# Kernel optimization log

Hardware: AMD Instinct MI355X
Metric: run time of the kernel (lower is better)

Reference implementation:

```python
import jax, jax.numpy as jnp
import numpy as np

B, C, H, W = 8, 256, 128, 128
N = H * W
TEMP = 0.07
NUM_NEG = 128
HARD_RADIUS = 4
HARD_RATIO = 0.75   # curriculum fully ramped (_current_hard_ratio == hard_ratio_max)
N_HARD = int(NUM_NEG * HARD_RATIO)   # 96
N_RAND = NUM_NEG - N_HARD            # 32
STEP = max(1, H // 16)               # 8
N_POS = ((H + STEP - 1) // STEP) * ((W + STEP - 1) // STEP)  # 256


def setup_inputs() -> dict:
    key = jax.random.key(0)
    ks = jax.random.split(key, 8)
    fmap_rgb = jax.random.normal(ks[0], (B, C, H, W), jnp.float32)
    fmap_depth = jax.random.normal(ks[1], (B, C, H, W), jnp.float32)
    pu = jax.random.uniform(ks[2], (B, H, W), jnp.float32) * (W - 1)
    pv = jax.random.uniform(ks[3], (B, H, W), jnp.float32) * (H - 1)
    projected_coords = jnp.stack([pu, pv], axis=1)  # (B,2,H,W)
    valid_mask = (jax.random.uniform(ks[4], (B, H, W)) < 0.9).astype(jnp.float32)
    rand_idx = jax.random.randint(ks[5], (B, N_RAND), 0, N, dtype=jnp.int32)
    hard_off_u = jax.random.randint(ks[6], (B, N_HARD, N_POS), -HARD_RADIUS, HARD_RADIUS + 1, dtype=jnp.int32)
    hard_off_v = jax.random.randint(ks[7], (B, N_HARD, N_POS), -HARD_RADIUS, HARD_RADIUS + 1, dtype=jnp.int32)
    return {
        'fmap_rgb': fmap_rgb, 'fmap_depth': fmap_depth,
        'projected_coords': projected_coords, 'valid_mask': valid_mask,
        'rand_idx': rand_idx, 'hard_off_u': hard_off_u, 'hard_off_v': hard_off_v,
    }


def _normalize(x):
    # F.normalize(dim=1): x / max(||x||_2, eps)
    n = jnp.sqrt(jnp.sum(x * x, axis=1, keepdims=True))
    return x / jnp.maximum(n, 1e-12)


def _bilinear_sample(f, x, y):
    # grid_sample(mode=bilinear, padding=zeros, align_corners=True); unnormalized
    # coords equal pixel coords (x=proj_u, y=proj_v). f:(B,C,H,W), x,y:(B,H,W) -> (B,C,N)
    Bb, Cc, Hh, Ww = f.shape
    ff = f.reshape(Bb, Cc, Hh * Ww)
    xf = x.reshape(Bb, -1)
    yf = y.reshape(Bb, -1)
    x0 = jnp.floor(xf)
    y0 = jnp.floor(yf)
    wx = xf - x0
    wy = yf - y0
    x0i = x0.astype(jnp.int32)
    y0i = y0.astype(jnp.int32)

    def g(ix, iy):
        valid = (ix >= 0) & (ix < Ww) & (iy >= 0) & (iy < Hh)
        idx = jnp.clip(iy, 0, Hh - 1) * Ww + jnp.clip(ix, 0, Ww - 1)
        v = jnp.take_along_axis(ff, idx[:, None, :], axis=2)
        return v * valid[:, None, :]

    return (((1 - wx) * (1 - wy))[:, None, :] * g(x0i, y0i)
            + (wx * (1 - wy))[:, None, :] * g(x0i + 1, y0i)
            + ((1 - wx) * wy)[:, None, :] * g(x0i, y0i + 1)
            + (wx * wy)[:, None, :] * g(x0i + 1, y0i + 1))


def reference(fmap_rgb, fmap_depth, projected_coords, valid_mask, rand_idx, hard_off_u, hard_off_v):
    rgb = _normalize(fmap_rgb)
    dep = _normalize(fmap_depth)
    proj_u = projected_coords[:, 0]
    proj_v = projected_coords[:, 1]

    rgb_pos = _bilinear_sample(rgb, proj_u, proj_v)        # (B,C,N)
    dep_flat = dep.reshape(B, C, N)
    rgb_flat = rgb.reshape(B, C, N)
    pos_sim = jnp.sum(dep_flat * rgb_pos, axis=1) / TEMP    # (B,N)

    # random negatives via gather + batched matmul
    rgb_rand = jnp.take_along_axis(rgb_flat, rand_idx[:, None, :].astype(jnp.int32), axis=2)  # (B,C,n_rand)
    rand_neg = jnp.einsum('bcn,bck->bkn', dep_flat, rgb_rand) / TEMP  # (B,n_rand,N)

    # hard negatives on coarse grid (step = H//16)
    gh = jnp.arange(0, H, STEP)
    gw = jnp.arange(0, W, STEP)
    ghf, gwf = [a.reshape(-1) for a in jnp.meshgrid(gh, gw, indexing='ij')]
    grid_idx = ghf * W + gwf                                # (n_pos,)
    pos_u = jnp.clip(proj_u[:, ghf, gwf], 0, W - 1).astype(jnp.int32)  # (B,n_pos)
    pos_v = jnp.clip(proj_v[:, ghf, gwf], 0, H - 1).astype(jnp.int32)
    off_u = jnp.where((hard_off_u == 0) & (hard_off_v == 0), 1, hard_off_u)
    hu = jnp.clip(pos_u[:, None, :] + off_u, 0, W - 1)      # (B,n_hard,n_pos)
    hv = jnp.clip(pos_v[:, None, :] + hard_off_v, 0, H - 1)
    hard_idx = (hv * W + hu).reshape(B, -1)                 # (B, n_hard*n_pos)
    rgb_hard = jnp.take_along_axis(rgb_flat, hard_idx[:, None, :], axis=2).reshape(B, C, N_HARD, N_POS)
    dep_grid = dep_flat[:, :, grid_idx]                     # (B,C,n_pos)
    hard_sim = jnp.einsum('bcp,bchp->bhp', dep_grid, rgb_hard) / TEMP  # (B,n_hard,n_pos)

    # logsumexp over [pos; random negs; hard negs] -- hard negs only exist at grid
    # positions (the torch code scatters into a dense -inf (B,n_hard,N) tensor;
    # logaddexp at grid positions is mathematically identical and avoids it).
    lse_base = jax.scipy.special.logsumexp(
        jnp.concatenate([pos_sim[:, None, :], rand_neg], axis=1), axis=1)  # (B,N)
    lse_hard = jax.scipy.special.logsumexp(hard_sim, axis=1)               # (B,n_pos)
    lse = lse_base.at[:, grid_idx].set(jnp.logaddexp(lse_base[:, grid_idx], lse_hard))

    mask = valid_mask.reshape(B, N)
    denom = jnp.maximum(jnp.sum(mask), 1.0)
    loss = jnp.sum((lse - pos_sim) * mask) / denom

    # accuracy (no_grad in torch); max over all negatives, hard ones only at grid idx
    max_neg = jnp.max(rand_neg, axis=1)
    max_neg = max_neg.at[:, grid_idx].max(jnp.max(hard_sim, axis=1))
    correct = ((pos_sim > max_neg) & (mask > 0.5)).astype(jnp.float32)
    accuracy = jnp.sum(correct) / denom * 100.0
    return loss, jax.lax.stop_gradient(accuracy)
```

## Files before the change

### kernel.cpp

```cpp
#include <hip/hip_runtime.h>
#include <cfloat>
#include <math.h>

#define B_ 8
#define C_ 256
#define C2_ (C_/2)
#define H_ 128
#define W_ 128
#define N_ (H_*W_)
#define NRAND 32
#define NHARD 96
#define NPOS 256
#define INV_TEMP (1.0f/0.07f)

typedef __attribute__((ext_vector_type(8))) short short8;
typedef __attribute__((ext_vector_type(4))) float f32x4;

__device__ __forceinline__ unsigned bf16rne(float x) {
    unsigned u = __float_as_uint(x);
    return (u + 0x7FFFu + ((u >> 16) & 1u)) >> 16;
}
__device__ __forceinline__ float blo(unsigned w) { return __uint_as_float(w << 16); }
__device__ __forceinline__ float bhi(unsigned w) { return __uint_as_float(w & 0xFFFF0000u); }

__global__ __launch_bounds__(256) void k1_rgb_norm_T(const float* __restrict__ rgb,
                                                     unsigned* __restrict__ rgbT) {
    __shared__ __align__(16) uint4 bounce[64 * 32];
    __shared__ float red[4][64];
    __shared__ float invn[64];
    int bi = blockIdx.x;
    int b  = bi >> 8;
    int p0 = (bi & 255) << 6;
    int t  = threadIdx.x;
    int lane = t & 63, w = t >> 6;

    const float* src = rgb + (size_t)b * C_ * N_ + p0 + lane;
    float v[64];
    float ssq = 0.f;
    #pragma unroll
    for (int k = 0; k < 64; ++k) {
        v[k] = src[(size_t)(w * 64 + k) * N_];
        ssq += v[k] * v[k];
    }
    red[w][lane] = ssq;
    __syncthreads();
    if (t < 64) {
        float s = red[0][t] + red[1][t] + red[2][t] + red[3][t];
        invn[t] = 1.0f / fmaxf(sqrtf(s), 1e-12f);
    }
    __syncthreads();
    float sc = invn[lane];
    int swz = lane & 7;
    #pragma unroll
    for (int j = 0; j < 8; ++j) {
        uint4 q;
        q.x = bf16rne(v[8 * j + 0] * sc) | (bf16rne(v[8 * j + 1] * sc) << 16);
        q.y = bf16rne(v[8 * j + 2] * sc) | (bf16rne(v[8 * j + 3] * sc) << 16);
        q.z = bf16rne(v[8 * j + 4] * sc) | (bf16rne(v[8 * j + 5] * sc) << 16);
        q.w = bf16rne(v[8 * j + 6] * sc) | (bf16rne(v[8 * j + 7] * sc) << 16);
        bounce[lane * 32 + ((w * 8 + j) ^ swz)] = q;
    }
    __syncthreads();
    uint4* dst = (uint4*)(rgbT + (size_t)(b * N_ + p0) * C2_);
    #pragma unroll
    for (int it = 0; it < 8; ++it) {
        int idx = it * 256 + t;
        int px = idx >> 5, j = idx & 31;
        dst[idx] = bounce[px * 32 + (j ^ (px & 7))];
    }
}

__global__ __launch_bounds__(256) void k2_main(
        const float* __restrict__ dep, const unsigned* __restrict__ rgbT,
        const float* __restrict__ coords, const int* __restrict__ rand_idx,
        float* __restrict__ lse_base, float* __restrict__ pos_out,
        float* __restrict__ maxneg_out, unsigned* __restrict__ depG) {
    __shared__ __align__(16) uint4 dep4[64 * 32];
    __shared__ __align__(16) uint4 rs4[32 * 32];
    __shared__ float red[4][64];
    __shared__ float invn[64];
    int bi = blockIdx.x;
    int b  = bi >> 8;
    int p0 = (bi & 255) << 6;
    int t  = threadIdx.x;
    int lane = t & 63, w = t >> 6;

    #pragma unroll
    for (int it = 0; it < 4; ++it) {
        int flat = it * 256 + t;
        int rn = flat >> 5, c8 = flat & 31;
        int idx = rand_idx[b * NRAND + rn];
        const uint4* src = (const uint4*)(rgbT + (size_t)(b * N_ + idx) * C2_);
        rs4[rn * 32 + (c8 ^ (rn & 7))] = src[c8];
    }

    const float* depb = dep + (size_t)b * C_ * N_ + p0 + lane;
    float ssq = 0.f;
    int psw = lane & 7;
    #pragma unroll 2
    for (int i = 0; i < 8; ++i) {
        int c0 = w * 64 + i * 8;
        float v[8];
        #pragma unroll
        for (int k = 0; k < 8; ++k) {
            v[k] = depb[(size_t)(c0 + k) * N_];
            ssq += v[k] * v[k];
        }
        uint4 q;
        q.x = bf16rne(v[0]) | (bf16rne(v[1]) << 16);
        q.y = bf16rne(v[2]) | (bf16rne(v[3]) << 16);
        q.z = bf16rne(v[4]) | (bf16rne(v[5]) << 16);
        q.w = bf16rne(v[6]) | (bf16rne(v[7]) << 16);
        dep4[lane * 32 + ((w * 8 + i) ^ psw)] = q;
    }
    red[w][lane] = ssq;

    int px = t >> 2, g = t & 3;
    int n  = p0 + px;
    float xf = coords[(size_t)b * 2 * N_ + n];
    float yf = coords[(size_t)b * 2 * N_ + N_ + n];
    float x0 = floorf(xf), y0 = floorf(yf);
    float wx = xf - x0, wy = yf - y0;
    int ix = (int)x0 + (g & 1);
    int iy = (int)y0 + (g >> 1);
    float wgt = ((g & 1) ? wx : 1.f - wx) * ((g & 2) ? wy : 1.f - wy);
    if (ix < 0 || ix >= W_ || iy < 0 || iy >= H_) wgt = 0.f;
    int ixc = min(max(ix, 0), W_ - 1), iyc = min(max(iy, 0), H_ - 1);
    const uint4* nbr4 = (const uint4*)(rgbT + (size_t)(b * N_ + iyc * W_ + ixc) * C2_);

    __syncthreads();
    if (t < 64) {
        float s = red[0][t] + red[1][t] + red[2][t] + red[3][t];
        invn[t] = 1.0f / fmaxf(sqrtf(s), 1e-12f);
    }

    f32x4 acc0 = {0.f, 0.f, 0.f, 0.f};
    f32x4 acc1 = {0.f, 0.f, 0.f, 0.f};
    int l15 = lane & 15, l4 = lane >> 4;
    int pxA = (w << 4) + l15;
    const short8* lds8 = (const short8*)dep4;
    const short8* rnd8 = (const short8*)rs4;
    #pragma unroll
    for (int kc = 0; kc < 8; ++kc) {
        int c8 = kc * 4 + l4;
        short8 a  = lds8[pxA * 32 + (c8 ^ (pxA & 7))];
        short8 b0 = rnd8[l15 * 32 + (c8 ^ (l15 & 7))];
        short8 b1 = rnd8[(16 + l15) * 32 + (c8 ^ (l15 & 7))];
        acc0 = __builtin_amdgcn_mfma_f32_16x16x32_bf16(a, b0, acc0, 0, 0, 0);
        acc1 = __builtin_amdgcn_mfma_f32_16x16x32_bf16(a, b1, acc1, 0, 0, 0);
    }

    float accN = 0.f;
    const uint4* drow = dep4 + (size_t)px * 32;
    int dsw = px & 7;
    #pragma unroll 4
    for (int c8 = 0; c8 < 32; ++c8) {
        uint4 dq = drow[c8 ^ dsw];
        uint4 rq = nbr4[c8];
        accN += blo(dq.x) * blo(rq.x) + bhi(dq.x) * bhi(rq.x)
              + blo(dq.y) * blo(rq.y) + bhi(dq.y) * bhi(rq.y)
              + blo(dq.z) * blo(rq.z) + bhi(dq.z) * bhi(rq.z)
              + blo(dq.w) * blo(rq.w) + bhi(dq.w) * bhi(rq.w);
    }
    __syncthreads();

    float* simsF = (float*)rs4;
    #pragma unroll
    for (int r = 0; r < 4; ++r) {
        int prow = (w << 4) + (l4 << 2) + r;
        int swn = r << 2;
        simsF[prow * 32 + (l15 ^ swn)]        = acc0[r];
        simsF[prow * 32 + (16 + (l15 ^ swn))] = acc1[r];
    }
    __syncthreads();

    float scale = invn[px] * INV_TEMP;
    float pp = accN * wgt;
    pp += __shfl_xor(pp, 1, 4);
    pp += __shfl_xor(pp, 2, 4);
    float pos = pp * scale;
    const float4* sf = (const float4*)simsF;
    int fsw = px & 3;
    float4 ra = sf[px * 8 + ((g * 2) ^ fsw)];
    float4 rb = sf[px * 8 + (((g * 2) ^ fsw) ^ 1)];
    float r[8] = {ra.x, ra.y, ra.z, ra.w, rb.x, rb.y, rb.z, rb.w};
    float ml = -FLT_MAX;
    #pragma unroll
    for (int j = 0; j < 8; ++j) { r[j] *= scale; ml = fmaxf(ml, r[j]); }
    ml = fmaxf(ml, __shfl_xor(ml, 1, 4));
    ml = fmaxf(ml, __shfl_xor(ml, 2, 4));
    float mneg = ml;
    float mall = fmaxf(mneg, pos);
    float se = 0.f;
    #pragma unroll
    for (int j = 0; j < 8; ++j) se += expf(r[j] - mall);
    se += __shfl_xor(se, 1, 4);
    se += __shfl_xor(se, 2, 4);
    if (g == 0) {
        float lse = mall + logf(se + expf(pos - mall));
        size_t o = (size_t)b * N_ + n;
        lse_base[o]   = lse;
        pos_out[o]    = pos;
        maxneg_out[o] = mneg;
    }

    int y = p0 >> 7;
    if ((y & 7) == 0) {
        int m = t >> 5, u = t & 31;
        int gpx = m * 8;
        int gx  = (p0 & 127) + gpx;
        int p   = ((y >> 3) << 4) + (gx >> 3);
        float sc = invn[gpx];
        const unsigned* srow = (const unsigned*)(dep4 + (size_t)gpx * 32);
        int xsw = (gpx & 7) << 2;
        unsigned* dst = depG + (size_t)((b << 8) + p) * 128;
        #pragma unroll
        for (int it = 0; it < 4; ++it) {
            int uu = u + it * 32;
            unsigned wv = srow[uu ^ xsw];
            dst[uu] = bf16rne(blo(wv) * sc) | (bf16rne(bhi(wv) * sc) << 16);
        }
    }
}

__global__ __launch_bounds__(192) void k3_hard(
        const unsigned* __restrict__ depG, const unsigned* __restrict__ rgbT,
        const float* __restrict__ coords, const int* __restrict__ hoffu,
        const int* __restrict__ hoffv, float* __restrict__ lse_hard,
        float* __restrict__ max_hard) {
    __shared__ __align__(16) float dv[256];
    __shared__ float sm_[3], ss_[3];
    int bp = blockIdx.x;
    int b = bp >> 8, p = bp & 255;
    int gy = (p >> 4) * 8, gx = (p & 15) * 8;
    int nn = gy * W_ + gx;
    int t  = threadIdx.x;
    if (t < 128) {
        unsigned wv = depG[(size_t)bp * 128 + t];
        dv[2 * t]     = blo(wv);
        dv[2 * t + 1] = bhi(wv);
    }
    float pu = coords[(size_t)b * 2 * N_ + nn];
    float pv = coords[(size_t)b * 2 * N_ + N_ + nn];
    int iu = (int)fminf(fmaxf(pu, 0.f), (float)(W_ - 1));
    int iv = (int)fminf(fmaxf(pv, 0.f), (float)(H_ - 1));
    int h = t >> 1, half = t & 1;
    int ou = hoffu[((size_t)b * NHARD + h) * NPOS + p];
    int ov = hoffv[((size_t)b * NHARD + h) * NPOS + p];
    __syncthreads();
    if (ou == 0 && ov == 0) ou = 1;
    int hu = min(max(iu + ou, 0), W_ - 1);
    int hv = min(max(iv + ov, 0), H_ - 1);
    const uint4* hvec = (const uint4*)(rgbT + (size_t)(b * N_ + hv * W_ + hu) * C2_)
                        + half * 16;
    const float4* dvv = (const float4*)dv + half * 32;
    float acc = 0.f;
    #pragma unroll 4
    for (int c8 = 0; c8 < 16; ++c8) {
        uint4 q = hvec[c8];
        float4 d0 = dvv[c8 * 2];
        float4 d1 = dvv[c8 * 2 + 1];
        acc += d0.x * blo(q.x) + d0.y * bhi(q.x)
             + d0.z * blo(q.y) + d0.w * bhi(q.y)
             + d1.x * blo(q.z) + d1.y * bhi(q.z)
             + d1.z * blo(q.w) + d1.w * bhi(q.w);
    }
    float sim = (acc + __shfl_xor(acc, 1, 2)) * INV_TEMP;
    float m = sim;
    #pragma unroll
    for (int o = 32; o > 0; o >>= 1) m = fmaxf(m, __shfl_xor(m, o, 64));
    int wid = t >> 6;
    if ((t & 63) == 0) sm_[wid] = m;
    __syncthreads();
    float mm = fmaxf(fmaxf(sm_[0], sm_[1]), sm_[2]);
    float e = (half == 0) ? expf(sim - mm) : 0.f;
    #pragma unroll
    for (int o = 32; o > 0; o >>= 1) e += __shfl_xor(e, o, 64);
    if ((t & 63) == 0) ss_[wid] = e;
    __syncthreads();
    if (t == 0) {
        lse_hard[bp] = mm + logf(ss_[0] + ss_[1] + ss_[2]);
        max_hard[bp] = mm;
    }
}

__global__ __launch_bounds__(256) void k4_reduce(
        const float* __restrict__ lse_base, const float* __restrict__ pos_sim,
        const float* __restrict__ max_neg, const float* __restrict__ mask,
        const float* __restrict__ lse_hard, const float* __restrict__ max_hard,
        float* __restrict__ acc) {
    int i = blockIdx.x * 256 + threadIdx.x;
    float l  = lse_base[i], ps = pos_sim[i], mn = max_neg[i], mk = mask[i];
    int b = i >> 14;
    int n = i & (N_ - 1);
    int y = n >> 7, x = n & 127;
    if (((y & 7) | (x & 7)) == 0) {
        int p = ((y >> 3) << 4) + (x >> 3);
        float lh = lse_hard[(b << 8) + p];
        float mh = max_hard[(b << 8) + p];
        float m = fmaxf(l, lh);
        l  = m + logf(expf(l - m) + expf(lh - m));
        mn = fmaxf(mn, mh);
    }
    float s0 = (l - ps) * mk;
    float s1 = (ps > mn && mk > 0.5f) ? 1.f : 0.f;
    float s2 = mk;
    #pragma unroll
    for (int o = 32; o > 0; o >>= 1) {
        s0 += __shfl_down(s0, o, 64);
        s1 += __shfl_down(s1, o, 64);
        s2 += __shfl_down(s2, o, 64);
    }
    __shared__ float r0[4], r1[4], r2[4];
    int wid = threadIdx.x >> 6;
    if ((threadIdx.x & 63) == 0) { r0[wid] = s0; r1[wid] = s1; r2[wid] = s2; }
    __syncthreads();
    if (threadIdx.x == 0) {
        atomicAdd(&acc[0], r0[0] + r0[1] + r0[2] + r0[3]);
        atomicAdd(&acc[1], r1[0] + r1[1] + r1[2] + r1[3]);
        atomicAdd(&acc[2], r2[0] + r2[1] + r2[2] + r2[3]);
    }
}

__global__ void k5_final(const float* __restrict__ acc, float* __restrict__ out) {
    if (threadIdx.x == 0) {
        float denom = fmaxf(acc[2], 1.0f);
        out[0] = acc[0] / denom;
        out[1] = acc[1] / denom * 100.0f;
    }
}

extern "C" void kernel_launch(void* const* d_in, const int* in_sizes, int n_in,
                              void* d_out, int out_size, void* d_ws, size_t ws_size,
                              hipStream_t stream) {
    const float* rgb     = (const float*)d_in[0];
    const float* dep     = (const float*)d_in[1];
    const float* coords  = (const float*)d_in[2];
    const float* mask    = (const float*)d_in[3];
    const int*   rand_i  = (const int*)d_in[4];
    const int*   hoffu   = (const int*)d_in[5];
    const int*   hoffv   = (const int*)d_in[6];
    float* out = (float*)d_out;
    char*  ws  = (char*)d_ws;

    const size_t RGBT_B = (size_t)B_ * N_ * C_ * 2;
    const size_t PIX_B  = (size_t)B_ * N_ * 4;
    unsigned* rgbT  = (unsigned*)ws;
    float* lse_base = (float*)(ws + RGBT_B);
    float* pos_sim  = (float*)(ws + RGBT_B + PIX_B);
    float* max_neg  = (float*)(ws + RGBT_B + 2 * PIX_B);
    float* lse_hard = (float*)(ws + RGBT_B + 3 * PIX_B);
    float* max_hard = (float*)(ws + RGBT_B + 3 * PIX_B + 8192);
    float* acc      = (float*)(ws + RGBT_B + 3 * PIX_B + 2 * 8192);
    unsigned* depG  = (unsigned*)(ws + RGBT_B + 3 * PIX_B + 2 * 8192 + 1024);

    hipMemsetAsync(acc, 0, 16, stream);
    k1_rgb_norm_T<<<B_ * (N_ / 64), 256, 0, stream>>>(rgb, rgbT);
    k2_main<<<B_ * (N_ / 64), 256, 0, stream>>>(dep, rgbT, coords, rand_i,
                                                lse_base, pos_sim, max_neg, depG);
    k3_hard<<<B_ * NPOS, 192, 0, stream>>>(depG, rgbT, coords, hoffu, hoffv,
                                           lse_hard, max_hard);
    k4_reduce<<<(B_ * N_) / 256, 256, 0, stream>>>(lse_base, pos_sim, max_neg,
                                                   mask, lse_hard, max_hard, acc);
    k5_final<<<1, 64, 0, stream>>>(acc, out);
}
```

Baseline: 371.8 us.

## Normalize depth features in first kernel and consume pre-transposed bf16 depth in main

```diff
diff --git a/kernel.cpp b/kernel.cpp
--- a/kernel.cpp
+++ b/kernel.cpp
@@ -23,18 +23,22 @@
 __device__ __forceinline__ float blo(unsigned w) { return __uint_as_float(w << 16); }
 __device__ __forceinline__ float bhi(unsigned w) { return __uint_as_float(w & 0xFFFF0000u); }
 
-__global__ __launch_bounds__(256) void k1_rgb_norm_T(const float* __restrict__ rgb,
-                                                     unsigned* __restrict__ rgbT) {
+__global__ __launch_bounds__(256, 4) void kA_norm(
+        const float* __restrict__ rgb, const float* __restrict__ dep,
+        unsigned* __restrict__ rgbT, unsigned* __restrict__ depT) {
     __shared__ __align__(16) uint4 bounce[64 * 32];
     __shared__ float red[4][64];
     __shared__ float invn[64];
     int bi = blockIdx.x;
-    int b  = bi >> 8;
-    int p0 = (bi & 255) << 6;
+    int srcsel = bi >> 11;
+    int sub = bi & 2047;
+    int b  = sub >> 8;
+    int p0 = (sub & 255) << 6;
     int t  = threadIdx.x;
     int lane = t & 63, w = t >> 6;
 
-    const float* src = rgb + (size_t)b * C_ * N_ + p0 + lane;
+    const float* src = (srcsel ? dep : rgb) + (size_t)b * C_ * N_ + p0 + lane;
+    unsigned* dstT = srcsel ? depT : rgbT;
     float v[64];
     float ssq = 0.f;
     #pragma unroll
@@ -61,7 +65,7 @@
         bounce[lane * 32 + ((w * 8 + j) ^ swz)] = q;
     }
     __syncthreads();
-    uint4* dst = (uint4*)(rgbT + (size_t)(b * N_ + p0) * C2_);
+    uint4* dst = (uint4*)(dstT + (size_t)(b * N_ + p0) * C2_);
     #pragma unroll
     for (int it = 0; it < 8; ++it) {
         int idx = it * 256 + t;
@@ -70,20 +74,18 @@
     }
 }
 
-__global__ __launch_bounds__(256) void k2_main(
-        const float* __restrict__ dep, const unsigned* __restrict__ rgbT,
+__global__ __launch_bounds__(256, 4) void k2_main(
+        const unsigned* __restrict__ depT, const unsigned* __restrict__ rgbT,
         const float* __restrict__ coords, const int* __restrict__ rand_idx,
         float* __restrict__ lse_base, float* __restrict__ pos_out,
-        float* __restrict__ maxneg_out, unsigned* __restrict__ depG) {
-    __shared__ __align__(16) uint4 dep4[64 * 32];
+        float* __restrict__ maxneg_out) {
     __shared__ __align__(16) uint4 rs4[32 * 32];
-    __shared__ float red[4][64];
-    __shared__ float invn[64];
     int bi = blockIdx.x;
     int b  = bi >> 8;
     int p0 = (bi & 255) << 6;
     int t  = threadIdx.x;
     int lane = t & 63, w = t >> 6;
+    int l15 = lane & 15, l4 = lane >> 4;
 
     #pragma unroll
     for (int it = 0; it < 4; ++it) {
@@ -94,26 +96,10 @@
         rs4[rn * 32 + (c8 ^ (rn & 7))] = src[c8];
     }
 
-    const float* depb = dep + (size_t)b * C_ * N_ + p0 + lane;
-    float ssq = 0.f;
-    int psw = lane & 7;
-    #pragma unroll 2
-    for (int i = 0; i < 8; ++i) {
-        int c0 = w * 64 + i * 8;
-        float v[8];
-        #pragma unroll
-        for (int k = 0; k < 8; ++k) {
-            v[k] = depb[(size_t)(c0 + k) * N_];
-            ssq += v[k] * v[k];
-        }
-        uint4 q;
-        q.x = bf16rne(v[0]) | (bf16rne(v[1]) << 16);
-        q.y = bf16rne(v[2]) | (bf16rne(v[3]) << 16);
-        q.z = bf16rne(v[4]) | (bf16rne(v[5]) << 16);
-        q.w = bf16rne(v[6]) | (bf16rne(v[7]) << 16);
-        dep4[lane * 32 + ((w * 8 + i) ^ psw)] = q;
-    }
-    red[w][lane] = ssq;
+    const short8* arow = (const short8*)(depT + (size_t)(b * N_ + p0 + (w << 4) + l15) * C2_);
+    short8 afr[8];
+    #pragma unroll
+    for (int kc = 0; kc < 8; ++kc) afr[kc] = arow[kc * 4 + l4];
 
     int px = t >> 2, g = t & 3;
     int n  = p0 + px;
@@ -129,33 +115,24 @@
     const uint4* nbr4 = (const uint4*)(rgbT + (size_t)(b * N_ + iyc * W_ + ixc) * C2_);
 
     __syncthreads();
-    if (t < 64) {
-        float s = red[0][t] + red[1][t] + red[2][t] + red[3][t];
-        invn[t] = 1.0f / fmaxf(sqrtf(s), 1e-12f);
-    }
 
     f32x4 acc0 = {0.f, 0.f, 0.f, 0.f};
     f32x4 acc1 = {0.f, 0.f, 0.f, 0.f};
-    int l15 = lane & 15, l4 = lane >> 4;
-    int pxA = (w << 4) + l15;
-    const short8* lds8 = (const short8*)dep4;
     const short8* rnd8 = (const short8*)rs4;
     #pragma unroll
     for (int kc = 0; kc < 8; ++kc) {
         int c8 = kc * 4 + l4;
-        short8 a  = lds8[pxA * 32 + (c8 ^ (pxA & 7))];
         short8 b0 = rnd8[l15 * 32 + (c8 ^ (l15 & 7))];
         short8 b1 = rnd8[(16 + l15) * 32 + (c8 ^ (l15 & 7))];
-        acc0 = __builtin_amdgcn_mfma_f32_16x16x32_bf16(a, b0, acc0, 0, 0, 0);
-        acc1 = __builtin_amdgcn_mfma_f32_16x16x32_bf16(a, b1, acc1, 0, 0, 0);
+        acc0 = __builtin_amdgcn_mfma_f32_16x16x32_bf16(afr[kc], b0, acc0, 0, 0, 0);
+        acc1 = __builtin_amdgcn_mfma_f32_16x16x32_bf16(afr[kc], b1, acc1, 0, 0, 0);
     }
 
     float accN = 0.f;
-    const uint4* drow = dep4 + (size_t)px * 32;
-    int dsw = px & 7;
+    const uint4* drow = (const uint4*)(depT + (size_t)(b * N_ + n) * C2_);
     #pragma unroll 4
     for (int c8 = 0; c8 < 32; ++c8) {
-        uint4 dq = drow[c8 ^ dsw];
+        uint4 dq = drow[c8];
         uint4 rq = nbr4[c8];
         accN += blo(dq.x) * blo(rq.x) + bhi(dq.x) * bhi(rq.x)
               + blo(dq.y) * blo(rq.y) + bhi(dq.y) * bhi(rq.y)
@@ -174,7 +151,7 @@
     }
     __syncthreads();
 
-    float scale = invn[px] * INV_TEMP;
+    const float scale = INV_TEMP;
     float pp = accN * wgt;
     pp += __shfl_xor(pp, 1, 4);
     pp += __shfl_xor(pp, 2, 4);
@@ -203,28 +180,10 @@
         pos_out[o]    = pos;
         maxneg_out[o] = mneg;
     }
-
-    int y = p0 >> 7;
-    if ((y & 7) == 0) {
-        int m = t >> 5, u = t & 31;
-        int gpx = m * 8;
-        int gx  = (p0 & 127) + gpx;
-        int p   = ((y >> 3) << 4) + (gx >> 3);
-        float sc = invn[gpx];
-        const unsigned* srow = (const unsigned*)(dep4 + (size_t)gpx * 32);
-        int xsw = (gpx & 7) << 2;
-        unsigned* dst = depG + (size_t)((b << 8) + p) * 128;
-        #pragma unroll
-        for (int it = 0; it < 4; ++it) {
-            int uu = u + it * 32;
-            unsigned wv = srow[uu ^ xsw];
-            dst[uu] = bf16rne(blo(wv) * sc) | (bf16rne(bhi(wv) * sc) << 16);
-        }
-    }
 }
 
 __global__ __launch_bounds__(192) void k3_hard(
-        const unsigned* __restrict__ depG, const unsigned* __restrict__ rgbT,
+        const unsigned* __restrict__ depT, const unsigned* __restrict__ rgbT,
         const float* __restrict__ coords, const int* __restrict__ hoffu,
         const int* __restrict__ hoffv, float* __restrict__ lse_hard,
         float* __restrict__ max_hard) {
@@ -236,7 +195,7 @@
     int nn = gy * W_ + gx;
     int t  = threadIdx.x;
     if (t < 128) {
-        unsigned wv = depG[(size_t)bp * 128 + t];
+        unsigned wv = depT[(size_t)(b * N_ + nn) * C2_ + t];
         dv[2 * t]     = blo(wv);
         dv[2 * t + 1] = bhi(wv);
     }
@@ -346,19 +305,19 @@
     const size_t RGBT_B = (size_t)B_ * N_ * C_ * 2;
     const size_t PIX_B  = (size_t)B_ * N_ * 4;
     unsigned* rgbT  = (unsigned*)ws;
-    float* lse_base = (float*)(ws + RGBT_B);
-    float* pos_sim  = (float*)(ws + RGBT_B + PIX_B);
-    float* max_neg  = (float*)(ws + RGBT_B + 2 * PIX_B);
-    float* lse_hard = (float*)(ws + RGBT_B + 3 * PIX_B);
-    float* max_hard = (float*)(ws + RGBT_B + 3 * PIX_B + 8192);
-    float* acc      = (float*)(ws + RGBT_B + 3 * PIX_B + 2 * 8192);
-    unsigned* depG  = (unsigned*)(ws + RGBT_B + 3 * PIX_B + 2 * 8192 + 1024);
+    unsigned* depT  = (unsigned*)(ws + RGBT_B);
+    float* lse_base = (float*)(ws + 2 * RGBT_B);
+    float* pos_sim  = (float*)(ws + 2 * RGBT_B + PIX_B);
+    float* max_neg  = (float*)(ws + 2 * RGBT_B + 2 * PIX_B);
+    float* lse_hard = (float*)(ws + 2 * RGBT_B + 3 * PIX_B);
+    float* max_hard = (float*)(ws + 2 * RGBT_B + 3 * PIX_B + 8192);
+    float* acc      = (float*)(ws + 2 * RGBT_B + 3 * PIX_B + 2 * 8192);
 
     hipMemsetAsync(acc, 0, 16, stream);
-    k1_rgb_norm_T<<<B_ * (N_ / 64), 256, 0, stream>>>(rgb, rgbT);
-    k2_main<<<B_ * (N_ / 64), 256, 0, stream>>>(dep, rgbT, coords, rand_i,
-                                                lse_base, pos_sim, max_neg, depG);
-    k3_hard<<<B_ * NPOS, 192, 0, stream>>>(depG, rgbT, coords, hoffu, hoffv,
+    kA_norm<<<2 * B_ * (N_ / 64), 256, 0, stream>>>(rgb, dep, rgbT, depT);
+    k2_main<<<B_ * (N_ / 64), 256, 0, stream>>>(depT, rgbT, coords, rand_i,
+                                                lse_base, pos_sim, max_neg);
+    k3_hard<<<B_ * NPOS, 192, 0, stream>>>(depT, rgbT, coords, hoffu, hoffv,
                                            lse_hard, max_hard);
     k4_reduce<<<(B_ * N_) / 256, 256, 0, stream>>>(lse_base, pos_sim, max_neg,
                                                    mask, lse_hard, max_hard, acc);
```

Measured after the change: 415.5 us. 11.7% more time.

## Fuse hard-negative scoring into main kernel and finalize via last-block reduction

Applied to the files above, without the earlier changes.

```diff
diff --git a/kernel.cpp b/kernel.cpp
--- a/kernel.cpp
+++ b/kernel.cpp
@@ -73,8 +73,10 @@
 __global__ __launch_bounds__(256) void k2_main(
         const float* __restrict__ dep, const unsigned* __restrict__ rgbT,
         const float* __restrict__ coords, const int* __restrict__ rand_idx,
+        const int* __restrict__ hoffu, const int* __restrict__ hoffv,
         float* __restrict__ lse_base, float* __restrict__ pos_out,
-        float* __restrict__ maxneg_out, unsigned* __restrict__ depG) {
+        float* __restrict__ maxneg_out, float* __restrict__ lse_hard,
+        float* __restrict__ max_hard) {
     __shared__ __align__(16) uint4 dep4[64 * 32];
     __shared__ __align__(16) uint4 rs4[32 * 32];
     __shared__ float red[4][64];
@@ -204,83 +206,64 @@
         maxneg_out[o] = mneg;
     }
 
-    int y = p0 >> 7;
-    if ((y & 7) == 0) {
-        int m = t >> 5, u = t & 31;
-        int gpx = m * 8;
-        int gx  = (p0 & 127) + gpx;
-        int p   = ((y >> 3) << 4) + (gx >> 3);
-        float sc = invn[gpx];
-        const unsigned* srow = (const unsigned*)(dep4 + (size_t)gpx * 32);
-        int xsw = (gpx & 7) << 2;
-        unsigned* dst = depG + (size_t)((b << 8) + p) * 128;
+    if (((bi & 255) & 14) == 0) {
+        int gp = t >> 5, wk = t & 31;
+        int y  = p0 >> 7;
+        int gx = (p0 & 127) + gp * 8;
+        int gpx = gp * 8;
+        int pidx = ((y >> 3) << 4) + (gx >> 3);
+        int nn = y * W_ + gx;
+        float pu = coords[(size_t)b * 2 * N_ + nn];
+        float pv = coords[(size_t)b * 2 * N_ + N_ + nn];
+        int iu = (int)fminf(fmaxf(pu, 0.f), (float)(W_ - 1));
+        int iv = (int)fminf(fmaxf(pv, 0.f), (float)(H_ - 1));
+        const uint4* hv0; const uint4* hv1; const uint4* hv2;
+        {
+            int h0 = wk, h1 = wk + 32, h2 = wk + 64;
+            int ou0 = hoffu[((size_t)b * NHARD + h0) * NPOS + pidx];
+            int ov0 = hoffv[((size_t)b * NHARD + h0) * NPOS + pidx];
+            int ou1 = hoffu[((size_t)b * NHARD + h1) * NPOS + pidx];
+            int ov1 = hoffv[((size_t)b * NHARD + h1) * NPOS + pidx];
+            int ou2 = hoffu[((size_t)b * NHARD + h2) * NPOS + pidx];
+            int ov2 = hoffv[((size_t)b * NHARD + h2) * NPOS + pidx];
+            if (ou0 == 0 && ov0 == 0) ou0 = 1;
+            if (ou1 == 0 && ov1 == 0) ou1 = 1;
+            if (ou2 == 0 && ov2 == 0) ou2 = 1;
+            int u0 = min(max(iu + ou0, 0), W_ - 1), v0 = min(max(iv + ov0, 0), H_ - 1);
+            int u1 = min(max(iu + ou1, 0), W_ - 1), v1 = min(max(iv + ov1, 0), H_ - 1);
+            int u2 = min(max(iu + ou2, 0), W_ - 1), v2 = min(max(iv + ov2, 0), H_ - 1);
+            hv0 = (const uint4*)(rgbT + (size_t)(b * N_ + v0 * W_ + u0) * C2_);
+            hv1 = (const uint4*)(rgbT + (size_t)(b * N_ + v1 * W_ + u1) * C2_);
+            hv2 = (const uint4*)(rgbT + (size_t)(b * N_ + v2 * W_ + u2) * C2_);
+        }
+        float a0 = 0.f, a1 = 0.f, a2 = 0.f;
+        const uint4* dr = dep4 + (size_t)gpx * 32;
+        int dsw2 = gpx & 7;
+        #pragma unroll 4
+        for (int c8 = 0; c8 < 32; ++c8) {
+            uint4 dq = dr[c8 ^ dsw2];
+            float d0 = blo(dq.x), d1 = bhi(dq.x), d2 = blo(dq.y), d3 = bhi(dq.y);
+            float d4 = blo(dq.z), d5 = bhi(dq.z), d6 = blo(dq.w), d7 = bhi(dq.w);
+            uint4 q0 = hv0[c8], q1 = hv1[c8], q2 = hv2[c8];
+            a0 += d0 * blo(q0.x) + d1 * bhi(q0.x) + d2 * blo(q0.y) + d3 * bhi(q0.y)
+                + d4 * blo(q0.z) + d5 * bhi(q0.z) + d6 * blo(q0.w) + d7 * bhi(q0.w);
+            a1 += d0 * blo(q1.x) + d1 * bhi(q1.x) + d2 * blo(q1.y) + d3 * bhi(q1.y)
+                + d4 * blo(q1.z) + d5 * bhi(q1.z) + d6 * blo(q1.w) + d7 * bhi(q1.w);
+            a2 += d0 * blo(q2.x) + d1 * bhi(q2.x) + d2 * blo(q2.y) + d3 * bhi(q2.y)
+                + d4 * blo(q2.z) + d5 * bhi(q2.z) + d6 * blo(q2.w) + d7 * bhi(q2.w);
+        }
+        float sc2 = invn[gpx] * INV_TEMP;
+        float s0v = a0 * sc2, s1v = a1 * sc2, s2v = a2 * sc2;
+        float ml2 = fmaxf(fmaxf(s0v, s1v), s2v);
         #pragma unroll
-        for (int it = 0; it < 4; ++it) {
-            int uu = u + it * 32;
-            unsigned wv = srow[uu ^ xsw];
-            dst[uu] = bf16rne(blo(wv) * sc) | (bf16rne(bhi(wv) * sc) << 16);
-        }
-    }
-}
-
-__global__ __launch_bounds__(192) void k3_hard(
-        const unsigned* __restrict__ depG, const unsigned* __restrict__ rgbT,
-        const float* __restrict__ coords, const int* __restrict__ hoffu,
-        const int* __restrict__ hoffv, float* __restrict__ lse_hard,
-        float* __restrict__ max_hard) {
-    __shared__ __align__(16) float dv[256];
-    __shared__ float sm_[3], ss_[3];
-    int bp = blockIdx.x;
-    int b = bp >> 8, p = bp & 255;
-    int gy = (p >> 4) * 8, gx = (p & 15) * 8;
-    int nn = gy * W_ + gx;
-    int t  = threadIdx.x;
-    if (t < 128) {
-        unsigned wv = depG[(size_t)bp * 128 + t];
-        dv[2 * t]     = blo(wv);
-        dv[2 * t + 1] = bhi(wv);
-    }
-    float pu = coords[(size_t)b * 2 * N_ + nn];
-    float pv = coords[(size_t)b * 2 * N_ + N_ + nn];
-    int iu = (int)fminf(fmaxf(pu, 0.f), (float)(W_ - 1));
-    int iv = (int)fminf(fmaxf(pv, 0.f), (float)(H_ - 1));
-    int h = t >> 1, half = t & 1;
-    int ou = hoffu[((size_t)b * NHARD + h) * NPOS + p];
-    int ov = hoffv[((size_t)b * NHARD + h) * NPOS + p];
-    __syncthreads();
-    if (ou == 0 && ov == 0) ou = 1;
-    int hu = min(max(iu + ou, 0), W_ - 1);
-    int hv = min(max(iv + ov, 0), H_ - 1);
-    const uint4* hvec = (const uint4*)(rgbT + (size_t)(b * N_ + hv * W_ + hu) * C2_)
-                        + half * 16;
-    const float4* dvv = (const float4*)dv + half * 32;
-    float acc = 0.f;
-    #pragma unroll 4
-    for (int c8 = 0; c8 < 16; ++c8) {
-        uint4 q = hvec[c8];
-        float4 d0 = dvv[c8 * 2];
-        float4 d1 = dvv[c8 * 2 + 1];
-        acc += d0.x * blo(q.x) + d0.y * bhi(q.x)
-             + d0.z * blo(q.y) + d0.w * bhi(q.y)
-             + d1.x * blo(q.z) + d1.y * bhi(q.z)
-             + d1.z * blo(q.w) + d1.w * bhi(q.w);
-    }
-    float sim = (acc + __shfl_xor(acc, 1, 2)) * INV_TEMP;
-    float m = sim;
-    #pragma unroll
-    for (int o = 32; o > 0; o >>= 1) m = fmaxf(m, __shfl_xor(m, o, 64));
-    int wid = t >> 6;
-    if ((t & 63) == 0) sm_[wid] = m;
-    __syncthreads();
-    float mm = fmaxf(fmaxf(sm_[0], sm_[1]), sm_[2]);
-    float e = (half == 0) ? expf(sim - mm) : 0.f;
-    #pragma unroll
-    for (int o = 32; o > 0; o >>= 1) e += __shfl_xor(e, o, 64);
-    if ((t & 63) == 0) ss_[wid] = e;
-    __syncthreads();
-    if (t == 0) {
-        lse_hard[bp] = mm + logf(ss_[0] + ss_[1] + ss_[2]);
-        max_hard[bp] = mm;
+        for (int o = 16; o > 0; o >>= 1) ml2 = fmaxf(ml2, __shfl_xor(ml2, o, 32));
+        float es = expf(s0v - ml2) + expf(s1v - ml2) + expf(s2v - ml2);
+        #pragma unroll
+        for (int o = 16; o > 0; o >>= 1) es += __shfl_xor(es, o, 32);
+        if (wk == 0) {
+            lse_hard[(b << 8) + pidx] = ml2 + logf(es);
+            max_hard[(b << 8) + pidx] = ml2;
+        }
     }
 }
 
@@ -288,7 +271,7 @@
         const float* __restrict__ lse_base, const float* __restrict__ pos_sim,
         const float* __restrict__ max_neg, const float* __restrict__ mask,
         const float* __restrict__ lse_hard, const float* __restrict__ max_hard,
-        float* __restrict__ acc) {
+        float* __restrict__ acc, float* __restrict__ out) {
     int i = blockIdx.x * 256 + threadIdx.x;
     float l  = lse_base[i], ps = pos_sim[i], mn = max_neg[i], mk = mask[i];
     int b = i >> 14;
@@ -319,14 +302,16 @@
         atomicAdd(&acc[0], r0[0] + r0[1] + r0[2] + r0[3]);
         atomicAdd(&acc[1], r1[0] + r1[1] + r1[2] + r1[3]);
         atomicAdd(&acc[2], r2[0] + r2[1] + r2[2] + r2[3]);
-    }
-}
-
-__global__ void k5_final(const float* __restrict__ acc, float* __restrict__ out) {
-    if (threadIdx.x == 0) {
-        float denom = fmaxf(acc[2], 1.0f);
-        out[0] = acc[0] / denom;
-        out[1] = acc[1] / denom * 100.0f;
+        __threadfence();
+        unsigned prev = atomicAdd((unsigned*)&acc[3], 1u);
+        if (prev == gridDim.x - 1) {
+            float t0 = atomicAdd(&acc[0], 0.f);
+            float t1 = atomicAdd(&acc[1], 0.f);
+            float t2 = atomicAdd(&acc[2], 0.f);
+            float denom = fmaxf(t2, 1.0f);
+            out[0] = t0 / denom;
+            out[1] = t1 / denom * 100.0f;
+        }
     }
 }
 
@@ -352,15 +337,13 @@
     float* lse_hard = (float*)(ws + RGBT_B + 3 * PIX_B);
     float* max_hard = (float*)(ws + RGBT_B + 3 * PIX_B + 8192);
     float* acc      = (float*)(ws + RGBT_B + 3 * PIX_B + 2 * 8192);
-    unsigned* depG  = (unsigned*)(ws + RGBT_B + 3 * PIX_B + 2 * 8192 + 1024);
 
     hipMemsetAsync(acc, 0, 16, stream);
     k1_rgb_norm_T<<<B_ * (N_ / 64), 256, 0, stream>>>(rgb, rgbT);
     k2_main<<<B_ * (N_ / 64), 256, 0, stream>>>(dep, rgbT, coords, rand_i,
-                                                lse_base, pos_sim, max_neg, depG);
-    k3_hard<<<B_ * NPOS, 192, 0, stream>>>(depG, rgbT, coords, hoffu, hoffv,
-                                           lse_hard, max_hard);
+                                                hoffu, hoffv, lse_base, pos_sim,
+                                                max_neg, lse_hard, max_hard);
     k4_reduce<<<(B_ * N_) / 256, 256, 0, stream>>>(lse_base, pos_sim, max_neg,
-                                                   mask, lse_hard, max_hard, acc);
-    k5_final<<<1, 64, 0, stream>>>(acc, out);
-}
+                                                   mask, lse_hard, max_hard,
+                                                   acc, out);
+}
```

New measurement: 446.4 us. 20.1% more time.

## Halve k2 pixel tile to 32 and fold final division into reduce kernel

Applied to the files above, without the earlier changes.

```diff
diff --git a/kernel.cpp b/kernel.cpp
--- a/kernel.cpp
+++ b/kernel.cpp
@@ -75,13 +75,13 @@
         const float* __restrict__ coords, const int* __restrict__ rand_idx,
         float* __restrict__ lse_base, float* __restrict__ pos_out,
         float* __restrict__ maxneg_out, unsigned* __restrict__ depG) {
-    __shared__ __align__(16) uint4 dep4[64 * 32];
+    __shared__ __align__(16) uint4 dep4[32 * 32];
     __shared__ __align__(16) uint4 rs4[32 * 32];
-    __shared__ float red[4][64];
-    __shared__ float invn[64];
+    __shared__ float red[8][32];
+    __shared__ float invn[32];
     int bi = blockIdx.x;
-    int b  = bi >> 8;
-    int p0 = (bi & 255) << 6;
+    int b  = bi >> 9;
+    int p0 = (bi & 511) << 5;
     int t  = threadIdx.x;
     int lane = t & 63, w = t >> 6;
 
@@ -94,12 +94,13 @@
         rs4[rn * 32 + (c8 ^ (rn & 7))] = src[c8];
     }
 
-    const float* depb = dep + (size_t)b * C_ * N_ + p0 + lane;
+    int px32 = t & 31, cg = t >> 5;
+    const float* depb = dep + (size_t)b * C_ * N_ + p0 + px32;
     float ssq = 0.f;
-    int psw = lane & 7;
+    int psw = px32 & 7;
     #pragma unroll 2
-    for (int i = 0; i < 8; ++i) {
-        int c0 = w * 64 + i * 8;
+    for (int i = 0; i < 4; ++i) {
+        int c0 = cg * 32 + i * 8;
         float v[8];
         #pragma unroll
         for (int k = 0; k < 8; ++k) {
@@ -111,11 +112,11 @@
         q.y = bf16rne(v[2]) | (bf16rne(v[3]) << 16);
         q.z = bf16rne(v[4]) | (bf16rne(v[5]) << 16);
         q.w = bf16rne(v[6]) | (bf16rne(v[7]) << 16);
-        dep4[lane * 32 + ((w * 8 + i) ^ psw)] = q;
-    }
-    red[w][lane] = ssq;
-
-    int px = t >> 2, g = t & 3;
+        dep4[px32 * 32 + ((cg * 4 + i) ^ psw)] = q;
+    }
+    red[cg][px32] = ssq;
+
+    int px = t >> 3, j = t & 7, g = j & 3, hc = j >> 2;
     int n  = p0 + px;
     float xf = coords[(size_t)b * 2 * N_ + n];
     float yf = coords[(size_t)b * 2 * N_ + N_ + n];
@@ -129,34 +130,36 @@
     const uint4* nbr4 = (const uint4*)(rgbT + (size_t)(b * N_ + iyc * W_ + ixc) * C2_);
 
     __syncthreads();
-    if (t < 64) {
-        float s = red[0][t] + red[1][t] + red[2][t] + red[3][t];
+    if (t < 32) {
+        float s = 0.f;
+        #pragma unroll
+        for (int gg = 0; gg < 8; ++gg) s += red[gg][t];
         invn[t] = 1.0f / fmaxf(sqrtf(s), 1e-12f);
     }
 
     f32x4 acc0 = {0.f, 0.f, 0.f, 0.f};
-    f32x4 acc1 = {0.f, 0.f, 0.f, 0.f};
     int l15 = lane & 15, l4 = lane >> 4;
-    int pxA = (w << 4) + l15;
+    int mh = w & 1, nh = w >> 1;
+    int arow = mh * 16 + l15;
+    int brow = nh * 16 + l15;
     const short8* lds8 = (const short8*)dep4;
     const short8* rnd8 = (const short8*)rs4;
     #pragma unroll
     for (int kc = 0; kc < 8; ++kc) {
         int c8 = kc * 4 + l4;
-        short8 a  = lds8[pxA * 32 + (c8 ^ (pxA & 7))];
-        short8 b0 = rnd8[l15 * 32 + (c8 ^ (l15 & 7))];
-        short8 b1 = rnd8[(16 + l15) * 32 + (c8 ^ (l15 & 7))];
+        short8 a  = lds8[arow * 32 + (c8 ^ (arow & 7))];
+        short8 b0 = rnd8[brow * 32 + (c8 ^ (brow & 7))];
         acc0 = __builtin_amdgcn_mfma_f32_16x16x32_bf16(a, b0, acc0, 0, 0, 0);
-        acc1 = __builtin_amdgcn_mfma_f32_16x16x32_bf16(a, b1, acc1, 0, 0, 0);
     }
 
     float accN = 0.f;
     const uint4* drow = dep4 + (size_t)px * 32;
     int dsw = px & 7;
     #pragma unroll 4
-    for (int c8 = 0; c8 < 32; ++c8) {
-        uint4 dq = drow[c8 ^ dsw];
-        uint4 rq = nbr4[c8];
+    for (int c = 0; c < 16; ++c) {
+        int cc = hc * 16 + c;
+        uint4 dq = drow[cc ^ dsw];
+        uint4 rq = nbr4[cc];
         accN += blo(dq.x) * blo(rq.x) + bhi(dq.x) * bhi(rq.x)
               + blo(dq.y) * blo(rq.y) + bhi(dq.y) * bhi(rq.y)
               + blo(dq.z) * blo(rq.z) + bhi(dq.z) * bhi(rq.z)
@@ -167,36 +170,37 @@
     float* simsF = (float*)rs4;
     #pragma unroll
     for (int r = 0; r < 4; ++r) {
-        int prow = (w << 4) + (l4 << 2) + r;
-        int swn = r << 2;
-        simsF[prow * 32 + (l15 ^ swn)]        = acc0[r];
-        simsF[prow * 32 + (16 + (l15 ^ swn))] = acc1[r];
+        int row = mh * 16 + (l4 << 2) + r;
+        int c   = nh * 16 + l15;
+        int f4  = (c >> 2) ^ (row & 7);
+        simsF[row * 32 + f4 * 4 + (c & 3)] = acc0[r];
     }
     __syncthreads();
 
     float scale = invn[px] * INV_TEMP;
     float pp = accN * wgt;
-    pp += __shfl_xor(pp, 1, 4);
-    pp += __shfl_xor(pp, 2, 4);
+    pp += __shfl_xor(pp, 1, 8);
+    pp += __shfl_xor(pp, 2, 8);
+    pp += __shfl_xor(pp, 4, 8);
     float pos = pp * scale;
     const float4* sf = (const float4*)simsF;
-    int fsw = px & 3;
-    float4 ra = sf[px * 8 + ((g * 2) ^ fsw)];
-    float4 rb = sf[px * 8 + (((g * 2) ^ fsw) ^ 1)];
-    float r[8] = {ra.x, ra.y, ra.z, ra.w, rb.x, rb.y, rb.z, rb.w};
+    float4 ra = sf[px * 8 + (j ^ (px & 7))];
+    float r4[4] = {ra.x, ra.y, ra.z, ra.w};
     float ml = -FLT_MAX;
     #pragma unroll
-    for (int j = 0; j < 8; ++j) { r[j] *= scale; ml = fmaxf(ml, r[j]); }
-    ml = fmaxf(ml, __shfl_xor(ml, 1, 4));
-    ml = fmaxf(ml, __shfl_xor(ml, 2, 4));
+    for (int e = 0; e < 4; ++e) { r4[e] *= scale; ml = fmaxf(ml, r4[e]); }
+    ml = fmaxf(ml, __shfl_xor(ml, 1, 8));
+    ml = fmaxf(ml, __shfl_xor(ml, 2, 8));
+    ml = fmaxf(ml, __shfl_xor(ml, 4, 8));
     float mneg = ml;
     float mall = fmaxf(mneg, pos);
     float se = 0.f;
     #pragma unroll
-    for (int j = 0; j < 8; ++j) se += expf(r[j] - mall);
-    se += __shfl_xor(se, 1, 4);
-    se += __shfl_xor(se, 2, 4);
-    if (g == 0) {
+    for (int e = 0; e < 4; ++e) se += expf(r4[e] - mall);
+    se += __shfl_xor(se, 1, 8);
+    se += __shfl_xor(se, 2, 8);
+    se += __shfl_xor(se, 4, 8);
+    if (j == 0) {
         float lse = mall + logf(se + expf(pos - mall));
         size_t o = (size_t)b * N_ + n;
         lse_base[o]   = lse;
@@ -206,18 +210,17 @@
 
     int y = p0 >> 7;
     if ((y & 7) == 0) {
-        int m = t >> 5, u = t & 31;
+        int m = t >> 6, u = t & 63;
         int gpx = m * 8;
         int gx  = (p0 & 127) + gpx;
         int p   = ((y >> 3) << 4) + (gx >> 3);
         float sc = invn[gpx];
         const unsigned* srow = (const unsigned*)(dep4 + (size_t)gpx * 32);
-        int xsw = (gpx & 7) << 2;
         unsigned* dst = depG + (size_t)((b << 8) + p) * 128;
         #pragma unroll
-        for (int it = 0; it < 4; ++it) {
-            int uu = u + it * 32;
-            unsigned wv = srow[uu ^ xsw];
+        for (int it = 0; it < 2; ++it) {
+            int uu = u + it * 64;
+            unsigned wv = srow[uu];
             dst[uu] = bf16rne(blo(wv) * sc) | (bf16rne(bhi(wv) * sc) << 16);
         }
     }
@@ -288,7 +291,7 @@
         const float* __restrict__ lse_base, const float* __restrict__ pos_sim,
         const float* __restrict__ max_neg, const float* __restrict__ mask,
         const float* __restrict__ lse_hard, const float* __restrict__ max_hard,
-        float* __restrict__ acc) {
+        float* __restrict__ acc, float* __restrict__ out) {
     int i = blockIdx.x * 256 + threadIdx.x;
     float l  = lse_base[i], ps = pos_sim[i], mn = max_neg[i], mk = mask[i];
     int b = i >> 14;
@@ -319,14 +322,16 @@
         atomicAdd(&acc[0], r0[0] + r0[1] + r0[2] + r0[3]);
         atomicAdd(&acc[1], r1[0] + r1[1] + r1[2] + r1[3]);
         atomicAdd(&acc[2], r2[0] + r2[1] + r2[2] + r2[3]);
-    }
-}
-
-__global__ void k5_final(const float* __restrict__ acc, float* __restrict__ out) {
-    if (threadIdx.x == 0) {
-        float denom = fmaxf(acc[2], 1.0f);
-        out[0] = acc[0] / denom;
-        out[1] = acc[1] / denom * 100.0f;
+        __threadfence();
+        unsigned prev = atomicAdd((unsigned*)&acc[3], 1u);
+        if (prev == gridDim.x - 1) {
+            float t0 = atomicAdd(&acc[0], 0.f);
+            float t1 = atomicAdd(&acc[1], 0.f);
+            float t2 = atomicAdd(&acc[2], 0.f);
+            float denom = fmaxf(t2, 1.0f);
+            out[0] = t0 / denom;
+            out[1] = t1 / denom * 100.0f;
+        }
     }
 }
 
@@ -356,11 +361,11 @@
 
     hipMemsetAsync(acc, 0, 16, stream);
     k1_rgb_norm_T<<<B_ * (N_ / 64), 256, 0, stream>>>(rgb, rgbT);
-    k2_main<<<B_ * (N_ / 64), 256, 0, stream>>>(dep, rgbT, coords, rand_i,
+    k2_main<<<B_ * (N_ / 32), 256, 0, stream>>>(dep, rgbT, coords, rand_i,
                                                 lse_base, pos_sim, max_neg, depG);
     k3_hard<<<B_ * NPOS, 192, 0, stream>>>(depG, rgbT, coords, hoffu, hoffv,
                                            lse_hard, max_hard);
     k4_reduce<<<(B_ * N_) / 256, 256, 0, stream>>>(lse_base, pos_sim, max_neg,
-                                                   mask, lse_hard, max_hard, acc);
-    k5_final<<<1, 64, 0, stream>>>(acc, out);
-}
+                                                   mask, lse_hard, max_hard,
+                                                   acc, out);
+}
```

Result: slower. 382.5 us (+2.9%).
